# Kernel optimization log

Measured on AMD Instinct MI355X. Metric: run time of the kernel, lower is better.

The kernel has to match this reference:

```python
import jax, jax.numpy as jnp
import numpy as np

N_STEPS = 128        # params['n_steps']
NOISE_SCALE = 0.01   # params['noise_scale']
DIMS_X = 16
HID = 512
BATCH = 32768
DIMS_IN = 2 * DIMS_X + 1  # cond_x1=True: cat([t, x_t, x_1])


def _linear_init(key, fan_in, fan_out):
    # torch nn.Linear default: U(-1/sqrt(fan_in), 1/sqrt(fan_in))
    bound = 1.0 / np.sqrt(fan_in)
    kw, kb = jax.random.split(key)
    w = jax.random.uniform(kw, (fan_in, fan_out), jnp.float32, -bound, bound)
    b = jax.random.uniform(kb, (fan_out,), jnp.float32, -bound, bound)
    return w, b


def setup_inputs() -> dict:
    key = jax.random.key(0)
    ks = jax.random.split(key, 6)
    w0, b0 = _linear_init(ks[0], DIMS_IN, HID)
    w1, b1 = _linear_init(ks[1], HID, HID)
    w2, b2 = _linear_init(ks[2], HID, HID)
    w3, b3 = _linear_init(ks[3], HID, HID)
    w4, b4 = _linear_init(ks[4], HID, DIMS_X)
    x_1 = jax.random.normal(ks[5], (BATCH, DIMS_X), jnp.float32)
    return {"x_1": x_1, "w0": w0, "b0": b0, "w1": w1, "b1": b1,
            "w2": w2, "b2": b2, "w3": w3, "b3": b3, "w4": w4, "b4": b4}


def reference(x_1, w0, b0, w1, b1, w2, b2, w3, b3, w4, b4):
    dtype = x_1.dtype
    steps = jnp.linspace(1.0, 0.0, N_STEPS).astype(dtype)
    t_arr = steps[:-1]       # t
    tprev_arr = steps[1:]    # tprev (< t)
    noise_key = jax.random.key(42)
    ones_col = jnp.ones((x_1.shape[0], 1), dtype)

    def net(t, x_t):
        h = jnp.concatenate([t * ones_col, x_t, x_1], axis=-1)  # [B, 2*Dx+1]
        for w, b in ((w0, b0), (w1, b1), (w2, b2), (w3, b3)):
            h = jax.nn.relu(h @ w + b)
        return h @ w4 + b4  # [B, Dx]

    def body(x_t, inp):
        t, tprev, i = inp
        drift = net(t, x_t)
        pred_x0 = x_t - t * drift
        x_new = (t - tprev) / t * pred_x0 + tprev / t * x_t
        noise = jax.random.normal(jax.random.fold_in(noise_key, i), x_t.shape, dtype)
        x_new = x_new + jnp.sqrt(NOISE_SCALE * tprev * (t - tprev) / t) * noise
        return x_new, None

    x0 = jax.lax.stop_gradient(x_1)  # x_t = x_1.detach()
    x_final, _ = jax.lax.scan(body, x0, (t_arr, tprev_arr, jnp.arange(N_STEPS - 1)))
    return x_final
```

## Files before the change

kernel.cpp:

```cpp
#include <hip/hip_runtime.h>

typedef _Float16 f16;
typedef __attribute__((ext_vector_type(4))) _Float16 f16x4;
typedef __attribute__((ext_vector_type(8))) _Float16 f16x8;
typedef __attribute__((ext_vector_type(4))) float f32x4;

#define HID 512
#define DIMS_X 16
#define NSTEPS 127
#define BM 128
#define BATCH 32768

#define OFF_W0 0
#define OFF_W1 32768
#define OFF_W2 (32768 + 262144)
#define OFF_W3 (32768 + 2 * 262144)
#define OFF_W4 (32768 + 3 * 262144)

__global__ void pack_w_kernel(const float* __restrict__ w, f16* __restrict__ out,
                              int K, int Kpad, int N) {
    int idx = blockIdx.x * blockDim.x + threadIdx.x;
    if (idx >= Kpad * N) return;
    int k = idx / N, n = idx - k * N;
    float v = (k < K) ? w[k * N + n] : 0.0f;
    out[(((k >> 3) * N) + n) * 8 + (k & 7)] = (f16)v;
}

__global__ void pack_w0_kernel(const float* __restrict__ w, f16* __restrict__ out) {
    int idx = blockIdx.x * blockDim.x + threadIdx.x;
    if (idx >= 64 * HID) return;
    int kn = idx / HID, n = idx - kn * HID;
    float v;
    if (kn < 32) v = w[(kn + 1) * HID + n];
    else if (kn == 32) v = w[n];
    else v = 0.0f;
    out[(((kn >> 3) * HID) + n) * 8 + (kn & 7)] = (f16)v;
}

__device__ __forceinline__ unsigned rotl32(unsigned x, int r) {
    return (x << r) | (x >> (32 - r));
}

__device__ __forceinline__ void threefry2x32(unsigned k0, unsigned k1,
                                             unsigned c0, unsigned c1,
                                             unsigned& o0, unsigned& o1) {
    unsigned ks2 = k0 ^ k1 ^ 0x1BD11BDAu;
    unsigned x0 = c0 + k0, x1 = c1 + k1;
#define TF_R(rot) { x0 += x1; x1 = rotl32(x1, rot); x1 ^= x0; }
    TF_R(13) TF_R(15) TF_R(26) TF_R(6)
    x0 += k1;  x1 += ks2 + 1u;
    TF_R(17) TF_R(29) TF_R(16) TF_R(24)
    x0 += ks2; x1 += k0 + 2u;
    TF_R(13) TF_R(15) TF_R(26) TF_R(6)
    x0 += k0;  x1 += k1 + 3u;
    TF_R(17) TF_R(29) TF_R(16) TF_R(24)
    x0 += k1;  x1 += ks2 + 4u;
    TF_R(13) TF_R(15) TF_R(26) TF_R(6)
    x0 += ks2; x1 += k0 + 5u;
#undef TF_R
    o0 = x0; o1 = x1;
}

__device__ __forceinline__ float erfinv_xla(float x) {
    float w = -log1pf(-x * x);
    float p;
    if (w < 5.0f) {
        w = w - 2.5f;
        p = 2.81022636e-08f;
        p = fmaf(p, w, 3.43273939e-07f);
        p = fmaf(p, w, -3.5233877e-06f);
        p = fmaf(p, w, -4.39150654e-06f);
        p = fmaf(p, w, 0.00021858087f);
        p = fmaf(p, w, -0.00125372503f);
        p = fmaf(p, w, -0.00417768164f);
        p = fmaf(p, w, 0.246640727f);
        p = fmaf(p, w, 1.50140941f);
    } else {
        w = sqrtf(w) - 3.0f;
        p = -0.000200214257f;
        p = fmaf(p, w, 0.000100950558f);
        p = fmaf(p, w, 0.00134934322f);
        p = fmaf(p, w, -0.00367342844f);
        p = fmaf(p, w, 0.00573950773f);
        p = fmaf(p, w, -0.0076224613f);
        p = fmaf(p, w, 0.00943887047f);
        p = fmaf(p, w, 1.00167406f);
        p = fmaf(p, w, 2.83297682f);
    }
    return p * x;
}

__device__ __forceinline__ unsigned lds_off(int row, int colByte) {
    return (unsigned)(row * 1024 + (colByte ^ ((row & 7) << 4)));
}

#define KC_BODY(kc, wc, wn, NKC)                                                      \
    {                                                                                 \
        if ((kc) + 1 < (NKC)) {                                                       \
            const f16* wk = wbase + (size_t)((kc) + 1) * (4 * HID * 8);               \
            wn[0] = *(const f16x8*)(wk);                                              \
            wn[1] = *(const f16x8*)(wk + 128);                                        \
            wn[2] = *(const f16x8*)(wk + 256);                                        \
            wn[3] = *(const f16x8*)(wk + 384);                                        \
        }                                                                             \
        f16x8 afr[8];                                                                 \
        _Pragma("unroll")                                                             \
        for (int tb = 0; tb < 8; ++tb)                                                \
            afr[tb] = *(const f16x8*)((const char*)act +                              \
                                      lds_off(tb * 16 + lc, (kc) * 64 + lk * 16));    \
        _Pragma("unroll")                                                             \
        for (int tn = 0; tn < 4; ++tn)                                                \
            _Pragma("unroll")                                                         \
            for (int tb = 0; tb < 8; ++tb)                                            \
                acc[tn][tb] = __builtin_amdgcn_mfma_f32_16x16x32_f16(                 \
                    wc[tn], afr[tb], acc[tn][tb], 0, 0, 0);                           \
    }

template <int NKC>
__device__ __forceinline__ void layer_swapped(f16* act, const f16* __restrict__ Wp,
                                              const float* bias_l,
                                              int wv, int lk, int lc) {
    f32x4 acc[4][8];
#pragma unroll
    for (int tn = 0; tn < 4; ++tn) {
        f32x4 bv = *(const f32x4*)(bias_l + wv * 64 + tn * 16 + lk * 4);
#pragma unroll
        for (int tb = 0; tb < 8; ++tb) acc[tn][tb] = bv;
    }

    const f16* wbase = Wp + ((size_t)lk * HID + wv * 64 + lc) * 8;
    f16x8 wA[4], wB[4];
    wA[0] = *(const f16x8*)(wbase);
    wA[1] = *(const f16x8*)(wbase + 128);
    wA[2] = *(const f16x8*)(wbase + 256);
    wA[3] = *(const f16x8*)(wbase + 384);

#pragma unroll 1
    for (int kp = 0; kp < NKC / 2; ++kp) {
        KC_BODY(2 * kp, wA, wB, NKC)
        KC_BODY(2 * kp + 1, wB, wA, NKC)
    }

    __syncthreads();
#pragma unroll
    for (int tn = 0; tn < 4; ++tn)
#pragma unroll
        for (int tb = 0; tb < 8; ++tb) {
            f16x4 v;
#pragma unroll
            for (int r = 0; r < 4; ++r) v[r] = (f16)fmaxf(acc[tn][tb][r], 0.0f);
            int brow = tb * 16 + lc;
            int nb = (wv * 64 + tn * 16 + lk * 4) * 2;
            *(f16x4*)((char*)act + lds_off(brow, nb)) = v;
        }
    __syncthreads();
}

__global__ __launch_bounds__(512, 2) void didi_main(
    const float* __restrict__ x1g,
    const float* __restrict__ b0g, const float* __restrict__ b1g,
    const float* __restrict__ b2g, const float* __restrict__ b3g,
    const float* __restrict__ b4g,
    const f16* __restrict__ wsp,
    float* __restrict__ outg) {
    __shared__ __align__(16) f16 act[BM * HID];
    __shared__ __align__(16) float bias_lds[4 * HID];

    const f16* W0p = wsp + OFF_W0;
    const f16* W1p = wsp + OFF_W1;
    const f16* W2p = wsp + OFF_W2;
    const f16* W3p = wsp + OFF_W3;
    const f16* W4p = wsp + OFF_W4;

    const int tid = threadIdx.x;
    const int wv = tid >> 6;
    const int ln = tid & 63;
    const int lk = ln >> 4;
    const int lc = ln & 15;
    const int rowBase = blockIdx.x * BM;

    for (int o = tid; o < HID; o += 512) {
        bias_lds[o] = b0g[o];
        bias_lds[HID + o] = b1g[o];
        bias_lds[2 * HID + o] = b2g[o];
        bias_lds[3 * HID + o] = b3g[o];
    }
    f32x4 bias4v = *(const f32x4*)(b4g + lk * 4);

    {
        f16x8 z = {};
        for (int o = tid; o < (BM * HID) / 8; o += 512)
            *(f16x8*)(act + o * 8) = z;
    }
    __syncthreads();

    f32x4 xr, x1r;
    {
        int grow = rowBase + wv * 16 + lc;
        x1r = *(const f32x4*)(x1g + grow * DIMS_X + lk * 4);
        xr = x1r;
        int lrow = wv * 16 + lc;
        f16x4 xf, x1f;
#pragma unroll
        for (int r = 0; r < 4; ++r) { xf[r] = (f16)xr[r]; x1f[r] = (f16)x1r[r]; }
        *(f16x4*)((char*)act + lds_off(lrow, lk * 8)) = xf;
        *(f16x4*)((char*)act + lds_off(lrow, 32 + lk * 8)) = x1f;
        if (lk == 0)
            *(f16*)((char*)act + lds_off(lrow, 64)) = (f16)1.0f;
    }
    __syncthreads();

    const float dstep = -1.0f / 127.0f;

#pragma unroll 1
    for (int i = 0; i < NSTEPS; ++i) {
        layer_swapped<2>(act, W0p, bias_lds, wv, lk, lc);
        layer_swapped<16>(act, W1p, bias_lds + HID, wv, lk, lc);
        layer_swapped<16>(act, W2p, bias_lds + 2 * HID, wv, lk, lc);
        layer_swapped<16>(act, W3p, bias_lds + 3 * HID, wv, lk, lc);

        float t  = 1.0f + (float)i * dstep;
        float tp = (i == NSTEPS - 1) ? 0.0f : 1.0f + (float)(i + 1) * dstep;

        {
            f32x4 acc4 = bias4v;
#pragma unroll 4
            for (int kc = 0; kc < 16; ++kc) {
                f16x8 w4fr = *(const f16x8*)(W4p + ((size_t)(kc * 4 + lk) * 16 + lc) * 8);
                f16x8 afr = *(const f16x8*)((const char*)act + lds_off(wv * 16 + lc, kc * 64 + lk * 16));
                acc4 = __builtin_amdgcn_mfma_f32_16x16x32_f16(w4fr, afr, acc4, 0, 0, 0);
            }
            float ca = (t - tp) / t;
            float cb = tp / t;
            float sig = sqrtf(((0.01f * tp) * (t - tp)) / t);
            unsigned fk0, fk1;
            threefry2x32(0u, 42u, 0u, (unsigned)i, fk0, fk1);
            int grow = rowBase + wv * 16 + lc;
            int lrow = wv * 16 + lc;
            f16x4 xf, x1f;
#pragma unroll
            for (int r = 0; r < 4; ++r) {
                float drift = acc4[r];
                unsigned flat = (unsigned)grow * 16u + (unsigned)(lk * 4 + r);
                unsigned o0, o1;
                threefry2x32(fk0, fk1, 0u, flat, o0, o1);
                unsigned bits = o0 ^ o1;
                float u01 = __uint_as_float((bits >> 9) | 0x3f800000u) - 1.0f;
                float u = u01 * 2.0f + (-0.99999994f);
                u = fmaxf(-0.99999994f, u);
                float nz = 1.4142135623730951f * erfinv_xla(u);
                float x = xr[r];
                float pred = x - t * drift;
                float xn = ca * pred + cb * x;
                xn = xn + sig * nz;
                xr[r] = xn;
                xf[r] = (f16)xn;
                x1f[r] = (f16)x1r[r];
            }
            *(f16x4*)((char*)act + lds_off(lrow, lk * 8)) = xf;
            *(f16x4*)((char*)act + lds_off(lrow, 32 + lk * 8)) = x1f;
            if (lk == 0)
                *(f16*)((char*)act + lds_off(lrow, 64)) = (f16)tp;
        }
        __syncthreads();
    }

    {
        int grow = rowBase + wv * 16 + lc;
        *(f32x4*)(outg + grow * DIMS_X + lk * 4) = xr;
    }
}

extern "C" void kernel_launch(void* const* d_in, const int* in_sizes, int n_in,
                              void* d_out, int out_size, void* d_ws, size_t ws_size,
                              hipStream_t stream) {
    const float* x1 = (const float*)d_in[0];
    const float* w0 = (const float*)d_in[1];
    const float* b0 = (const float*)d_in[2];
    const float* w1 = (const float*)d_in[3];
    const float* b1 = (const float*)d_in[4];
    const float* w2 = (const float*)d_in[5];
    const float* b2 = (const float*)d_in[6];
    const float* w3 = (const float*)d_in[7];
    const float* b3 = (const float*)d_in[8];
    const float* w4 = (const float*)d_in[9];
    const float* b4 = (const float*)d_in[10];
    f16* ws = (f16*)d_ws;

    hipLaunchKernelGGL(pack_w0_kernel, dim3(128), dim3(256), 0, stream, w0, ws + OFF_W0);
    hipLaunchKernelGGL(pack_w_kernel, dim3(1024), dim3(256), 0, stream, w1, ws + OFF_W1, 512, 512, 512);
    hipLaunchKernelGGL(pack_w_kernel, dim3(1024), dim3(256), 0, stream, w2, ws + OFF_W2, 512, 512, 512);
    hipLaunchKernelGGL(pack_w_kernel, dim3(1024), dim3(256), 0, stream, w3, ws + OFF_W3, 512, 512, 512);
    hipLaunchKernelGGL(pack_w_kernel, dim3(32), dim3(256), 0, stream, w4, ws + OFF_W4, 512, 512, 16);

    hipLaunchKernelGGL(didi_main, dim3(BATCH / BM), dim3(512), 0, stream,
                       x1, b0, b1, b2, b3, b4, (const f16*)ws, (float*)d_out);
}
```

Measured before the change: 5.692 ms.

## Switch hidden-layer GEMMs from 16x16x32 to 32x32x16 MFMA tiles

The hidden-layer matmuls now use 32x32x16 f16 MFMA instructions instead of 16x16x32 ones. Fragment indexing, bias broadcast, weight prefetch stride and the LDS XOR swizzle (now keyed on row&31) are reworked to match the 32-row tiles. Each wave issues fewer, larger MFMAs for the same work, aiming for higher matrix-core efficiency and less issue overhead. The wider swizzle changes LDS bank-conflict behaviour for the output-layer reads, which still use the 16x16 layout.

```diff
diff --git a/kernel.cpp b/kernel.cpp
--- a/kernel.cpp
+++ b/kernel.cpp
@@ -4,6 +4,7 @@
 typedef __attribute__((ext_vector_type(4))) _Float16 f16x4;
 typedef __attribute__((ext_vector_type(8))) _Float16 f16x8;
 typedef __attribute__((ext_vector_type(4))) float f32x4;
+typedef __attribute__((ext_vector_type(16))) float f32x16;
 
 #define HID 512
 #define DIMS_X 16
@@ -91,67 +92,75 @@
 }
 
 __device__ __forceinline__ unsigned lds_off(int row, int colByte) {
-    return (unsigned)(row * 1024 + (colByte ^ ((row & 7) << 4)));
-}
-
-#define KC_BODY(kc, wc, wn, NKC)                                                      \
+    return (unsigned)(row * 1024 + (colByte ^ ((row & 31) << 4)));
+}
+
+#define KC_BODY(kc, wc, wn, NCHUNK)                                                   \
     {                                                                                 \
-        if ((kc) + 1 < (NKC)) {                                                       \
-            const f16* wk = wbase + (size_t)((kc) + 1) * (4 * HID * 8);               \
+        if ((kc) + 1 < (NCHUNK)) {                                                    \
+            const f16* wk = wbase + (size_t)((kc) + 1) * (2 * HID * 8);               \
             wn[0] = *(const f16x8*)(wk);                                              \
-            wn[1] = *(const f16x8*)(wk + 128);                                        \
-            wn[2] = *(const f16x8*)(wk + 256);                                        \
-            wn[3] = *(const f16x8*)(wk + 384);                                        \
+            wn[1] = *(const f16x8*)(wk + 256);                                        \
         }                                                                             \
-        f16x8 afr[8];                                                                 \
+        f16x8 bfr[4];                                                                 \
         _Pragma("unroll")                                                             \
-        for (int tb = 0; tb < 8; ++tb)                                                \
-            afr[tb] = *(const f16x8*)((const char*)act +                              \
-                                      lds_off(tb * 16 + lc, (kc) * 64 + lk * 16));    \
+        for (int tb = 0; tb < 4; ++tb)                                                \
+            bfr[tb] = *(const f16x8*)((const char*)act +                              \
+                                      lds_off(tb * 32 + l31, (kc) * 32 + kh * 16));   \
         _Pragma("unroll")                                                             \
-        for (int tn = 0; tn < 4; ++tn)                                                \
+        for (int t = 0; t < 2; ++t)                                                   \
             _Pragma("unroll")                                                         \
-            for (int tb = 0; tb < 8; ++tb)                                            \
-                acc[tn][tb] = __builtin_amdgcn_mfma_f32_16x16x32_f16(                 \
-                    wc[tn], afr[tb], acc[tn][tb], 0, 0, 0);                           \
-    }
-
-template <int NKC>
+            for (int tb = 0; tb < 4; ++tb)                                            \
+                acc[t][tb] = __builtin_amdgcn_mfma_f32_32x32x16_f16(                  \
+                    wc[t], bfr[tb], acc[t][tb], 0, 0, 0);                             \
+    }
+
+template <int NCHUNK>
 __device__ __forceinline__ void layer_swapped(f16* act, const f16* __restrict__ Wp,
                                               const float* bias_l,
-                                              int wv, int lk, int lc) {
-    f32x4 acc[4][8];
-#pragma unroll
-    for (int tn = 0; tn < 4; ++tn) {
-        f32x4 bv = *(const f32x4*)(bias_l + wv * 64 + tn * 16 + lk * 4);
-#pragma unroll
-        for (int tb = 0; tb < 8; ++tb) acc[tn][tb] = bv;
-    }
-
-    const f16* wbase = Wp + ((size_t)lk * HID + wv * 64 + lc) * 8;
-    f16x8 wA[4], wB[4];
+                                              int wv, int l31, int kh) {
+    f32x16 acc[2][4];
+#pragma unroll
+    for (int t = 0; t < 2; ++t) {
+        f32x4 bq0 = *(const f32x4*)(bias_l + wv * 64 + t * 32 + 0 + kh * 4);
+        f32x4 bq1 = *(const f32x4*)(bias_l + wv * 64 + t * 32 + 8 + kh * 4);
+        f32x4 bq2 = *(const f32x4*)(bias_l + wv * 64 + t * 32 + 16 + kh * 4);
+        f32x4 bq3 = *(const f32x4*)(bias_l + wv * 64 + t * 32 + 24 + kh * 4);
+        f32x16 bv;
+#pragma unroll
+        for (int r = 0; r < 4; ++r) {
+            bv[r] = bq0[r]; bv[4 + r] = bq1[r]; bv[8 + r] = bq2[r]; bv[12 + r] = bq3[r];
+        }
+#pragma unroll
+        for (int tb = 0; tb < 4; ++tb) acc[t][tb] = bv;
+    }
+
+    const f16* wbase = Wp + ((size_t)kh * HID + wv * 64 + l31) * 8;
+    f16x8 wA[2], wB[2];
     wA[0] = *(const f16x8*)(wbase);
-    wA[1] = *(const f16x8*)(wbase + 128);
-    wA[2] = *(const f16x8*)(wbase + 256);
-    wA[3] = *(const f16x8*)(wbase + 384);
+    wA[1] = *(const f16x8*)(wbase + 256);
 
 #pragma unroll 1
-    for (int kp = 0; kp < NKC / 2; ++kp) {
-        KC_BODY(2 * kp, wA, wB, NKC)
-        KC_BODY(2 * kp + 1, wB, wA, NKC)
+    for (int kp = 0; kp < NCHUNK / 2; ++kp) {
+        KC_BODY(2 * kp, wA, wB, NCHUNK)
+        KC_BODY(2 * kp + 1, wB, wA, NCHUNK)
     }
 
     __syncthreads();
 #pragma unroll
-    for (int tn = 0; tn < 4; ++tn)
-#pragma unroll
-        for (int tb = 0; tb < 8; ++tb) {
-            f16x4 v;
-#pragma unroll
-            for (int r = 0; r < 4; ++r) v[r] = (f16)fmaxf(acc[tn][tb][r], 0.0f);
-            int brow = tb * 16 + lc;
-            int nb = (wv * 64 + tn * 16 + lk * 4) * 2;
-            *(f16x4*)((char*)act + lds_off(brow, nb)) = v;
+    for (int t = 0; t < 2; ++t)
+#pragma unroll
+        for (int tb = 0; tb < 4; ++tb) {
+            int b = tb * 32 + l31;
+#pragma unroll
+            for (int q = 0; q < 4; ++q) {
+                f16x4 v;
+#pragma unroll
+                for (int r = 0; r < 4; ++r)
+                    v[r] = (f16)fmaxf(acc[t][tb][4 * q + r], 0.0f);
+                int nb = (wv * 64 + t * 32 + q * 8 + kh * 4) * 2;
+                *(f16x4*)((char*)act + lds_off(b, nb)) = v;
+            }
         }
     __syncthreads();
 }
@@ -175,6 +184,8 @@
     const int tid = threadIdx.x;
     const int wv = tid >> 6;
     const int ln = tid & 63;
+    const int l31 = ln & 31;
+    const int kh = ln >> 5;
     const int lk = ln >> 4;
     const int lc = ln & 15;
     const int rowBase = blockIdx.x * BM;
@@ -214,10 +225,10 @@
 
 #pragma unroll 1
     for (int i = 0; i < NSTEPS; ++i) {
-        layer_swapped<2>(act, W0p, bias_lds, wv, lk, lc);
-        layer_swapped<16>(act, W1p, bias_lds + HID, wv, lk, lc);
-        layer_swapped<16>(act, W2p, bias_lds + 2 * HID, wv, lk, lc);
-        layer_swapped<16>(act, W3p, bias_lds + 3 * HID, wv, lk, lc);
+        layer_swapped<4>(act, W0p, bias_lds, wv, l31, kh);
+        layer_swapped<32>(act, W1p, bias_lds + HID, wv, l31, kh);
+        layer_swapped<32>(act, W2p, bias_lds + 2 * HID, wv, l31, kh);
+        layer_swapped<32>(act, W3p, bias_lds + 3 * HID, wv, l31, kh);
 
         float t  = 1.0f + (float)i * dstep;
         float tp = (i == NSTEPS - 1) ? 0.0f : 1.0f + (float)(i + 1) * dstep;
```

Result: slower. 5.983 ms (+5.1%).
